# Optimization experiments

Measured on AMD Instinct MI355X. Metric: run time of the kernel, lower is better.

## Reference

```python
import jax, jax.numpy as jnp
import numpy as np

B, T, C = 512, 256, 384   # batch, seq (== block_size), n_embd
HS, BS = 64, 256          # head_size, block_size


def setup_inputs() -> dict:
    key = jax.random.key(0)
    ks = jax.random.split(key, 6)
    s = 1.0 / np.sqrt(C)
    s2 = 1.0 / np.sqrt(HS)
    return {
        "x": jax.random.normal(ks[0], (B, T, C), jnp.float32),
        "W_q": jax.random.normal(ks[1], (C, HS), jnp.float32) * s,
        "W_k": jax.random.normal(ks[2], (C, HS), jnp.float32) * s,
        "W_v": jax.random.normal(ks[3], (C, HS), jnp.float32) * s,
        "W_ql": jax.random.normal(ks[4], (HS, BS), jnp.float32) * s2,
        "W_kl": jax.random.normal(ks[5], (HS, BS), jnp.float32) * s2,
    }


def reference(x, W_q, W_k, W_v, W_ql, W_kl):
    # One head of self-attention, additive (tanh) score variant, eval mode.
    # x: [B,T,C]
    q = jnp.einsum("btc,ch->bth", x, W_q)          # [B,T,HS]
    k = jnp.einsum("btc,ch->bth", x, W_k)          # [B,T,HS]
    q_w = jnp.einsum("bth,hs->bts", q, W_ql)       # [B,T,BS]
    k_w = jnp.einsum("bth,hs->bts", k, W_kl)       # [B,T,BS]
    # NOTE: elementwise add (both [B,T,BS]) as in the torch code, then tanh.
    wei = jnp.tanh(q_w + k_w)                      # [B,T,T] since T == BS
    Tn = x.shape[1]
    causal = jnp.tril(jnp.ones((Tn, Tn), dtype=bool))
    wei = jnp.where(causal, wei, -jnp.inf)
    wei = jax.nn.softmax(wei, axis=-1)
    v = jnp.einsum("btc,ch->bth", x, W_v)          # [B,T,HS]
    out = jnp.einsum("bts,bsh->bth", wei, v)       # [B,T,HS]
    return out
```

## Files before the change

kernel.cpp:

```cpp
#include <hip/hip_runtime.h>

#define BATCH 512
#define TT    256
#define CC    384
#define HH    64

typedef float  f32x4 __attribute__((ext_vector_type(4)));
typedef short  s16x8 __attribute__((ext_vector_type(8)));

#define VB_OFF    0
#define SCR_OFF   32768
#define LDS_TOTAL 131072

__device__ __forceinline__ unsigned short f2bf(float f) {
    union { float f; unsigned u; } c; c.f = f;
    unsigned u = c.u;
    u += 0x7fffu + ((u >> 16) & 1u);
    return (unsigned short)(u >> 16);
}

__device__ __forceinline__ s16x8 cvt8(float4 f0, float4 f1) {
    s16x8 v;
    v[0] = (short)f2bf(f0.x); v[1] = (short)f2bf(f0.y);
    v[2] = (short)f2bf(f0.z); v[3] = (short)f2bf(f0.w);
    v[4] = (short)f2bf(f1.x); v[5] = (short)f2bf(f1.y);
    v[6] = (short)f2bf(f1.z); v[7] = (short)f2bf(f1.w);
    return v;
}

__global__ void prep_w(const float* __restrict__ Wq, const float* __restrict__ Wk,
                       const float* __restrict__ Wv, const float* __restrict__ Wql,
                       const float* __restrict__ Wkl, unsigned short* __restrict__ wsW) {
    int gid = blockIdx.x * 256 + threadIdx.x;
    int k, n; float val;
    if (gid < CC * 256) {
        k = gid >> 8; int s = gid & 255; n = s;
        float acc = 0.f;
        for (int h = 0; h < HH; ++h)
            acc += Wq[k * HH + h] * Wql[h * 256 + s] + Wk[k * HH + h] * Wkl[h * 256 + s];
        val = acc;
    } else {
        int g2 = gid - CC * 256;
        k = g2 >> 6; int h = g2 & 63; n = 256 + h;
        val = Wv[k * HH + h];
    }
    int kk2 = k >> 5, ct = n >> 4;
    int lane = ((k >> 3) & 3) * 16 + (n & 15);
    int j = k & 7;
    wsW[(((kk2 * 20 + ct) * 64) + lane) * 8 + j] = f2bf(val);
}

__global__ __launch_bounds__(512, 2) void head_main(const float* __restrict__ x,
                                                    const unsigned short* __restrict__ wsW,
                                                    float* __restrict__ out) {
    extern __shared__ char sm[];
    unsigned short* Vb  = (unsigned short*)(sm + VB_OFF);

    const int t    = threadIdx.x;
    const int w    = (t >> 6) & 7;
    const int lane = t & 63;
    const int q    = lane >> 4;
    const int cidx = lane & 15;
    const int rt0  = w;
    const int rt1  = 15 - w;
    unsigned short* scr = (unsigned short*)(sm + SCR_OFF + w * 12288);

    const float* xb  = x + (size_t)blockIdx.x * (TT * CC);
    const float* xa0 = xb + (rt0 * 16 + cidx) * CC + q * 8;
    const float* xa1 = xb + (rt1 * 16 + cidx) * CC + q * 8;

    f32x4 accV[2][4];
#pragma unroll
    for (int i = 0; i < 2; ++i)
#pragma unroll
        for (int j = 0; j < 4; ++j) accV[i][j] = (f32x4){0.f,0.f,0.f,0.f};
    {
        float4 p00 = *(const float4*)(xa0),     p01 = *(const float4*)(xa0 + 4);
        float4 p10 = *(const float4*)(xa1),     p11 = *(const float4*)(xa1 + 4);
        for (int kk = 0; kk < 12; ++kk) {
            s16x8 a0 = cvt8(p00, p01), a1 = cvt8(p10, p11);
            if (kk < 11) {
                const float* n0 = xa0 + (kk + 1) * 32;
                const float* n1 = xa1 + (kk + 1) * 32;
                p00 = *(const float4*)(n0); p01 = *(const float4*)(n0 + 4);
                p10 = *(const float4*)(n1); p11 = *(const float4*)(n1 + 4);
            }
            const unsigned short* wb = wsW + (size_t)kk * 10240 + 16 * 512 + lane * 8;
            s16x8 b0 = *(const s16x8*)(wb);
            s16x8 b1 = *(const s16x8*)(wb + 512);
            s16x8 b2 = *(const s16x8*)(wb + 1024);
            s16x8 b3 = *(const s16x8*)(wb + 1536);
            accV[0][0] = __builtin_amdgcn_mfma_f32_16x16x32_bf16(a0, b0, accV[0][0], 0, 0, 0);
            accV[1][0] = __builtin_amdgcn_mfma_f32_16x16x32_bf16(a1, b0, accV[1][0], 0, 0, 0);
            accV[0][1] = __builtin_amdgcn_mfma_f32_16x16x32_bf16(a0, b1, accV[0][1], 0, 0, 0);
            accV[1][1] = __builtin_amdgcn_mfma_f32_16x16x32_bf16(a1, b1, accV[1][1], 0, 0, 0);
            accV[0][2] = __builtin_amdgcn_mfma_f32_16x16x32_bf16(a0, b2, accV[0][2], 0, 0, 0);
            accV[1][2] = __builtin_amdgcn_mfma_f32_16x16x32_bf16(a1, b2, accV[1][2], 0, 0, 0);
            accV[0][3] = __builtin_amdgcn_mfma_f32_16x16x32_bf16(a0, b3, accV[0][3], 0, 0, 0);
            accV[1][3] = __builtin_amdgcn_mfma_f32_16x16x32_bf16(a1, b3, accV[1][3], 0, 0, 0);
        }
    }
#pragma unroll
    for (int ri = 0; ri < 2; ++ri) {
        const int rt = ri ? rt1 : rt0;
#pragma unroll
        for (int vct = 0; vct < 4; ++vct)
#pragma unroll
            for (int rg = 0; rg < 4; ++rg) {
                int srow = rt * 16 + q * 4 + rg;
                Vb[((vct * 8 + (srow >> 5)) * 64 + ((srow >> 3) & 3) * 16 + cidx) * 8 + (srow & 7)] =
                    f2bf(accV[ri][vct][rg]);
            }
    }

    f32x4 accS1[16], accS0[8];
#pragma unroll
    for (int i = 0; i < 16; ++i) accS1[i] = (f32x4){0.f,0.f,0.f,0.f};
#pragma unroll
    for (int i = 0; i < 8; ++i)  accS0[i] = (f32x4){0.f,0.f,0.f,0.f};

    const bool ng4   = (rt1 >= 12);
    const bool g0two = (rt0 >= 4);
    {
        float4 p00 = *(const float4*)(xa0),     p01 = *(const float4*)(xa0 + 4);
        float4 p10 = *(const float4*)(xa1),     p11 = *(const float4*)(xa1 + 4);
        for (int kk = 0; kk < 12; ++kk) {
            s16x8 a0 = cvt8(p00, p01), a1 = cvt8(p10, p11);
            if (kk < 11) {
                const float* n0 = xa0 + (kk + 1) * 32;
                const float* n1 = xa1 + (kk + 1) * 32;
                p00 = *(const float4*)(n0); p01 = *(const float4*)(n0 + 4);
                p10 = *(const float4*)(n1); p11 = *(const float4*)(n1 + 4);
            }
            const unsigned short* wb = wsW + (size_t)kk * 10240 + lane * 8;
            s16x8 bfA[4], bfB[4];
#pragma unroll
            for (int i = 0; i < 4; ++i) bfA[i] = *(const s16x8*)(wb + i * 512);
#pragma unroll
            for (int i = 0; i < 4; ++i) bfB[i] = *(const s16x8*)(wb + (4 + i) * 512);
#pragma unroll
            for (int i = 0; i < 4; ++i) {
                accS1[i] = __builtin_amdgcn_mfma_f32_16x16x32_bf16(a1, bfA[i], accS1[i], 0, 0, 0);
                accS0[i] = __builtin_amdgcn_mfma_f32_16x16x32_bf16(a0, bfA[i], accS0[i], 0, 0, 0);
            }
#pragma unroll
            for (int i = 0; i < 4; ++i) bfA[i] = *(const s16x8*)(wb + (8 + i) * 512);
#pragma unroll
            for (int i = 0; i < 4; ++i)
                accS1[4 + i] = __builtin_amdgcn_mfma_f32_16x16x32_bf16(a1, bfB[i], accS1[4 + i], 0, 0, 0);
            if (g0two) {
#pragma unroll
                for (int i = 0; i < 4; ++i)
                    accS0[4 + i] = __builtin_amdgcn_mfma_f32_16x16x32_bf16(a0, bfB[i], accS0[4 + i], 0, 0, 0);
            }
            if (ng4) {
#pragma unroll
                for (int i = 0; i < 4; ++i) bfB[i] = *(const s16x8*)(wb + (12 + i) * 512);
            }
#pragma unroll
            for (int i = 0; i < 4; ++i)
                accS1[8 + i] = __builtin_amdgcn_mfma_f32_16x16x32_bf16(a1, bfA[i], accS1[8 + i], 0, 0, 0);
            if (ng4) {
#pragma unroll
                for (int i = 0; i < 4; ++i)
                    accS1[12 + i] = __builtin_amdgcn_mfma_f32_16x16x32_bf16(a1, bfB[i], accS1[12 + i], 0, 0, 0);
            }
        }
    }

    float rs0[4] = {0.f,0.f,0.f,0.f}, rs1[4] = {0.f,0.f,0.f,0.f};
    s16x8 pf0[4], pf1[8];
    const int nch1 = rt1 >> 1;
    const int nch0 = rt0 >> 1;

#pragma unroll
    for (int ch = 0; ch < 8; ++ch) {
        if (ch <= nch1) {
#pragma unroll
            for (int sub = 0; sub < 2; ++sub) {
                const int ct = 2 * ch + sub;
                const int gcol = ct * 16 + cidx;
                const int c = sub * 16 + cidx;
#pragma unroll
                for (int rg = 0; rg < 4; ++rg) {
                    const int grow = rt1 * 16 + q * 4 + rg;
                    float e = 0.f;
                    if (ct <= rt1 && gcol <= grow) {
                        float sv = accS1[ct][rg];
                        float ex = __expf(2.f * sv);
                        float th = 1.f - __fdividef(2.f, ex + 1.f);
                        e = __expf(th);
                    }
                    rs1[rg] += e;
                    scr[ch * 512 + ((c >> 3) * 16 + q * 4 + rg) * 8 + (c & 7)] = f2bf(e);
                }
            }
        }
    }
#pragma unroll
    for (int ch = 0; ch < 8; ++ch)
        if (ch <= nch1) pf1[ch] = *(const s16x8*)(scr + ch * 512 + lane * 8);

#pragma unroll
    for (int ch = 0; ch < 4; ++ch) {
        if (ch <= nch0) {
#pragma unroll
            for (int sub = 0; sub < 2; ++sub) {
                const int ct = 2 * ch + sub;
                const int gcol = ct * 16 + cidx;
                const int c = sub * 16 + cidx;
#pragma unroll
                for (int rg = 0; rg < 4; ++rg) {
                    const int grow = rt0 * 16 + q * 4 + rg;
                    float e = 0.f;
                    if (ct <= rt0 && gcol <= grow) {
                        float sv = accS0[ct][rg];
                        float ex = __expf(2.f * sv);
                        float th = 1.f - __fdividef(2.f, ex + 1.f);
                        e = __expf(th);
                    }
                    rs0[rg] += e;
                    scr[4096 + ch * 512 + ((c >> 3) * 16 + q * 4 + rg) * 8 + (c & 7)] = f2bf(e);
                }
            }
        }
    }
#pragma unroll
    for (int ch = 0; ch < 4; ++ch)
        if (ch <= nch0) pf0[ch] = *(const s16x8*)(scr + 4096 + ch * 512 + lane * 8);

#pragma unroll
    for (int rg = 0; rg < 4; ++rg) {
        float v0 = rs0[rg], v1 = rs1[rg];
        v0 += __shfl_xor(v0, 1); v0 += __shfl_xor(v0, 2);
        v0 += __shfl_xor(v0, 4); v0 += __shfl_xor(v0, 8);
        v1 += __shfl_xor(v1, 1); v1 += __shfl_xor(v1, 2);
        v1 += __shfl_xor(v1, 4); v1 += __shfl_xor(v1, 8);
        rs0[rg] = v0; rs1[rg] = v1;
    }

    __syncthreads();

    f32x4 acc2[2][4];
#pragma unroll
    for (int i = 0; i < 2; ++i)
#pragma unroll
        for (int j = 0; j < 4; ++j) acc2[i][j] = (f32x4){0.f,0.f,0.f,0.f};

#pragma unroll
    for (int ch = 0; ch < 8; ++ch) {
        if (ch <= nch1) {
            s16x8 vb[4];
#pragma unroll
            for (int vct = 0; vct < 4; ++vct)
                vb[vct] = *(const s16x8*)(Vb + ((vct * 8 + ch) * 64 + lane) * 8);
#pragma unroll
            for (int vct = 0; vct < 4; ++vct)
                acc2[1][vct] = __builtin_amdgcn_mfma_f32_16x16x32_bf16(pf1[ch], vb[vct], acc2[1][vct], 0, 0, 0);
            if (ch < 4 && ch <= nch0) {
#pragma unroll
                for (int vct = 0; vct < 4; ++vct)
                    acc2[0][vct] = __builtin_amdgcn_mfma_f32_16x16x32_bf16(pf0[ch], vb[vct], acc2[0][vct], 0, 0, 0);
            }
        }
    }

    float* ob = out + (size_t)blockIdx.x * (TT * HH);
#pragma unroll
    for (int ri = 0; ri < 2; ++ri) {
        const int rt = ri ? rt1 : rt0;
#pragma unroll
        for (int rg = 0; rg < 4; ++rg) {
            int row = rt * 16 + q * 4 + rg;
            float inv = __fdividef(1.f, ri ? rs1[rg] : rs0[rg]);
#pragma unroll
            for (int vct = 0; vct < 4; ++vct)
                ob[row * HH + vct * 16 + cidx] = acc2[ri][vct][rg] * inv;
        }
    }
}

extern "C" void kernel_launch(void* const* d_in, const int* in_sizes, int n_in,
                              void* d_out, int out_size, void* d_ws, size_t ws_size,
                              hipStream_t stream) {
    const float* x   = (const float*)d_in[0];
    const float* Wq  = (const float*)d_in[1];
    const float* Wk  = (const float*)d_in[2];
    const float* Wv  = (const float*)d_in[3];
    const float* Wql = (const float*)d_in[4];
    const float* Wkl = (const float*)d_in[5];
    unsigned short* wsW = (unsigned short*)d_ws;
    float* out = (float*)d_out;

    prep_w<<<480, 256, 0, stream>>>(Wq, Wk, Wv, Wql, Wkl, wsW);

    hipFuncSetAttribute((const void*)head_main,
                        hipFuncAttributeMaxDynamicSharedMemorySize, LDS_TOTAL);
    head_main<<<BATCH, 512, LDS_TOTAL, stream>>>(x, wsW, out);
}
```

Measured before the change: 361.4 us.

## Merge score accumulators, shrink LDS scratch, raise occupancy to four blocks per CU

Both row tiles now share one 18-entry score accumulator array, with the short row tile packed into the slots the long tile leaves unused, so fewer accumulator registers are live. Per-wave scratch shrinks to a two-slot ping-pong buffer and total LDS falls from 128KB to 48KB, so launch bounds can target four 512-thread blocks per CU. MFMAs for tiles entirely above the causal diagonal are skipped per tile. The trade-offs are more LDS round trips and possible register spills under the tighter register budget.

```diff
diff --git a/kernel.cpp b/kernel.cpp
--- a/kernel.cpp
+++ b/kernel.cpp
@@ -10,7 +10,7 @@
 
 #define VB_OFF    0
 #define SCR_OFF   32768
-#define LDS_TOTAL 131072
+#define LDS_TOTAL 49152
 
 __device__ __forceinline__ unsigned short f2bf(float f) {
     union { float f; unsigned u; } c; c.f = f;
@@ -50,7 +50,7 @@
     wsW[(((kk2 * 20 + ct) * 64) + lane) * 8 + j] = f2bf(val);
 }
 
-__global__ __launch_bounds__(512, 2) void head_main(const float* __restrict__ x,
+__global__ __launch_bounds__(512, 4) void head_main(const float* __restrict__ x,
                                                     const unsigned short* __restrict__ wsW,
                                                     float* __restrict__ out) {
     extern __shared__ char sm[];
@@ -63,7 +63,9 @@
     const int cidx = lane & 15;
     const int rt0  = w;
     const int rt1  = 15 - w;
-    unsigned short* scr = (unsigned short*)(sm + SCR_OFF + w * 12288);
+    const int nt0  = rt0 + 2 - (rt0 & 1);
+    const int jbase = 18 - nt0;
+    unsigned short* scr = (unsigned short*)(sm + SCR_OFF) + w * 1024;
 
     const float* xb  = x + (size_t)blockIdx.x * (TT * CC);
     const float* xa0 = xb + (rt0 * 16 + cidx) * CC + q * 8;
@@ -75,8 +77,8 @@
 #pragma unroll
         for (int j = 0; j < 4; ++j) accV[i][j] = (f32x4){0.f,0.f,0.f,0.f};
     {
-        float4 p00 = *(const float4*)(xa0),     p01 = *(const float4*)(xa0 + 4);
-        float4 p10 = *(const float4*)(xa1),     p11 = *(const float4*)(xa1 + 4);
+        float4 p00 = *(const float4*)(xa0), p01 = *(const float4*)(xa0 + 4);
+        float4 p10 = *(const float4*)(xa1), p11 = *(const float4*)(xa1 + 4);
         for (int kk = 0; kk < 12; ++kk) {
             s16x8 a0 = cvt8(p00, p01), a1 = cvt8(p10, p11);
             if (kk < 11) {
@@ -113,17 +115,13 @@
             }
     }
 
-    f32x4 accS1[16], accS0[8];
-#pragma unroll
-    for (int i = 0; i < 16; ++i) accS1[i] = (f32x4){0.f,0.f,0.f,0.f};
-#pragma unroll
-    for (int i = 0; i < 8; ++i)  accS0[i] = (f32x4){0.f,0.f,0.f,0.f};
-
-    const bool ng4   = (rt1 >= 12);
-    const bool g0two = (rt0 >= 4);
+    f32x4 accS[18];
+#pragma unroll
+    for (int i = 0; i < 18; ++i) accS[i] = (f32x4){0.f,0.f,0.f,0.f};
+
     {
-        float4 p00 = *(const float4*)(xa0),     p01 = *(const float4*)(xa0 + 4);
-        float4 p10 = *(const float4*)(xa1),     p11 = *(const float4*)(xa1 + 4);
+        float4 p00 = *(const float4*)(xa0), p01 = *(const float4*)(xa0 + 4);
+        float4 p10 = *(const float4*)(xa1), p11 = *(const float4*)(xa1 + 4);
         for (int kk = 0; kk < 12; ++kk) {
             s16x8 a0 = cvt8(p00, p01), a1 = cvt8(p10, p11);
             if (kk < 11) {
@@ -133,37 +131,38 @@
                 p10 = *(const float4*)(n1); p11 = *(const float4*)(n1 + 4);
             }
             const unsigned short* wb = wsW + (size_t)kk * 10240 + lane * 8;
-            s16x8 bfA[4], bfB[4];
-#pragma unroll
-            for (int i = 0; i < 4; ++i) bfA[i] = *(const s16x8*)(wb + i * 512);
-#pragma unroll
-            for (int i = 0; i < 4; ++i) bfB[i] = *(const s16x8*)(wb + (4 + i) * 512);
-#pragma unroll
-            for (int i = 0; i < 4; ++i) {
-                accS1[i] = __builtin_amdgcn_mfma_f32_16x16x32_bf16(a1, bfA[i], accS1[i], 0, 0, 0);
-                accS0[i] = __builtin_amdgcn_mfma_f32_16x16x32_bf16(a0, bfA[i], accS0[i], 0, 0, 0);
-            }
-#pragma unroll
-            for (int i = 0; i < 4; ++i) bfA[i] = *(const s16x8*)(wb + (8 + i) * 512);
+            s16x8 bf[4];
+#pragma unroll
+            for (int i = 0; i < 4; ++i) bf[i] = *(const s16x8*)(wb + i * 512);
 #pragma unroll
             for (int i = 0; i < 4; ++i)
-                accS1[4 + i] = __builtin_amdgcn_mfma_f32_16x16x32_bf16(a1, bfB[i], accS1[4 + i], 0, 0, 0);
-            if (g0two) {
+                accS[i] = __builtin_amdgcn_mfma_f32_16x16x32_bf16(a1, bf[i], accS[i], 0, 0, 0);
+#pragma unroll
+            for (int i = 0; i < 4; ++i) bf[i] = *(const s16x8*)(wb + (4 + i) * 512);
+#pragma unroll
+            for (int i = 0; i < 4; ++i)
+                accS[4 + i] = __builtin_amdgcn_mfma_f32_16x16x32_bf16(a1, bf[i], accS[4 + i], 0, 0, 0);
+#pragma unroll
+            for (int i = 0; i < 4; ++i) bf[i] = *(const s16x8*)(wb + (8 + i) * 512);
+#pragma unroll
+            for (int i = 0; i < 4; ++i)
+                if (8 + i <= rt1)
+                    accS[8 + i] = __builtin_amdgcn_mfma_f32_16x16x32_bf16(a1, bf[i], accS[8 + i], 0, 0, 0);
+            if (rt1 >= 12) {
+#pragma unroll
+                for (int i = 0; i < 4; ++i) bf[i] = *(const s16x8*)(wb + (12 + i) * 512);
 #pragma unroll
                 for (int i = 0; i < 4; ++i)
-                    accS0[4 + i] = __builtin_amdgcn_mfma_f32_16x16x32_bf16(a0, bfB[i], accS0[4 + i], 0, 0, 0);
-            }
-            if (ng4) {
-#pragma unroll
-                for (int i = 0; i < 4; ++i) bfB[i] = *(const s16x8*)(wb + (12 + i) * 512);
-            }
-#pragma unroll
-            for (int i = 0; i < 4; ++i)
-                accS1[8 + i] = __builtin_amdgcn_mfma_f32_16x16x32_bf16(a1, bfA[i], accS1[8 + i], 0, 0, 0);
-            if (ng4) {
-#pragma unroll
-                for (int i = 0; i < 4; ++i)
-                    accS1[12 + i] = __builtin_amdgcn_mfma_f32_16x16x32_bf16(a1, bfB[i], accS1[12 + i], 0, 0, 0);
+                    if (12 + i <= rt1)
+                        accS[12 + i] = __builtin_amdgcn_mfma_f32_16x16x32_bf16(a1, bf[i], accS[12 + i], 0, 0, 0);
+            }
+            const unsigned short* wb0 = wb - jbase * 512;
+#pragma unroll
+            for (int j = 10; j < 18; ++j) {
+                if (j >= jbase) {
+                    s16x8 b = *(const s16x8*)(wb0 + j * 512);
+                    accS[j] = __builtin_amdgcn_mfma_f32_16x16x32_bf16(a0, b, accS[j], 0, 0, 0);
+                }
             }
         }
     }
@@ -171,11 +170,11 @@
     float rs0[4] = {0.f,0.f,0.f,0.f}, rs1[4] = {0.f,0.f,0.f,0.f};
     s16x8 pf0[4], pf1[8];
     const int nch1 = rt1 >> 1;
-    const int nch0 = rt0 >> 1;
 
 #pragma unroll
     for (int ch = 0; ch < 8; ++ch) {
         if (ch <= nch1) {
+            unsigned short* reg = scr + (ch & 1) * 512;
 #pragma unroll
             for (int sub = 0; sub < 2; ++sub) {
                 const int ct = 2 * ch + sub;
@@ -186,48 +185,46 @@
                     const int grow = rt1 * 16 + q * 4 + rg;
                     float e = 0.f;
                     if (ct <= rt1 && gcol <= grow) {
-                        float sv = accS1[ct][rg];
+                        float sv = accS[ct][rg];
                         float ex = __expf(2.f * sv);
                         float th = 1.f - __fdividef(2.f, ex + 1.f);
                         e = __expf(th);
                     }
                     rs1[rg] += e;
-                    scr[ch * 512 + ((c >> 3) * 16 + q * 4 + rg) * 8 + (c & 7)] = f2bf(e);
+                    reg[((c >> 3) * 16 + q * 4 + rg) * 8 + (c & 7)] = f2bf(e);
                 }
             }
-        }
-    }
-#pragma unroll
-    for (int ch = 0; ch < 8; ++ch)
-        if (ch <= nch1) pf1[ch] = *(const s16x8*)(scr + ch * 512 + lane * 8);
-
-#pragma unroll
-    for (int ch = 0; ch < 4; ++ch) {
-        if (ch <= nch0) {
+            pf1[ch] = *(const s16x8*)(reg + lane * 8);
+        }
+    }
+#pragma unroll
+    for (int s = 0; s < 4; ++s) {
+        const int je = 10 + 2 * s;
+        if (je >= jbase) {
+            const int ch0 = (je - jbase) >> 1;
+            unsigned short* reg = scr + (s & 1) * 512;
 #pragma unroll
             for (int sub = 0; sub < 2; ++sub) {
-                const int ct = 2 * ch + sub;
-                const int gcol = ct * 16 + cidx;
+                const int ct0 = 2 * ch0 + sub;
+                const int gcol = ct0 * 16 + cidx;
                 const int c = sub * 16 + cidx;
 #pragma unroll
                 for (int rg = 0; rg < 4; ++rg) {
                     const int grow = rt0 * 16 + q * 4 + rg;
                     float e = 0.f;
-                    if (ct <= rt0 && gcol <= grow) {
-                        float sv = accS0[ct][rg];
+                    if (ct0 <= rt0 && gcol <= grow) {
+                        float sv = accS[je + sub][rg];
                         float ex = __expf(2.f * sv);
                         float th = 1.f - __fdividef(2.f, ex + 1.f);
                         e = __expf(th);
                     }
                     rs0[rg] += e;
-                    scr[4096 + ch * 512 + ((c >> 3) * 16 + q * 4 + rg) * 8 + (c & 7)] = f2bf(e);
+                    reg[((c >> 3) * 16 + q * 4 + rg) * 8 + (c & 7)] = f2bf(e);
                 }
             }
-        }
-    }
-#pragma unroll
-    for (int ch = 0; ch < 4; ++ch)
-        if (ch <= nch0) pf0[ch] = *(const s16x8*)(scr + 4096 + ch * 512 + lane * 8);
+            pf0[s] = *(const s16x8*)(reg + lane * 8);
+        }
+    }
 
 #pragma unroll
     for (int rg = 0; rg < 4; ++rg) {
@@ -257,11 +254,19 @@
 #pragma unroll
             for (int vct = 0; vct < 4; ++vct)
                 acc2[1][vct] = __builtin_amdgcn_mfma_f32_16x16x32_bf16(pf1[ch], vb[vct], acc2[1][vct], 0, 0, 0);
-            if (ch < 4 && ch <= nch0) {
-#pragma unroll
-                for (int vct = 0; vct < 4; ++vct)
-                    acc2[0][vct] = __builtin_amdgcn_mfma_f32_16x16x32_bf16(pf0[ch], vb[vct], acc2[0][vct], 0, 0, 0);
-            }
+        }
+    }
+#pragma unroll
+    for (int s = 0; s < 4; ++s) {
+        if (10 + 2 * s >= jbase) {
+            const int ch0 = s - ((jbase - 10) >> 1);
+            s16x8 vb[4];
+#pragma unroll
+            for (int vct = 0; vct < 4; ++vct)
+                vb[vct] = *(const s16x8*)(Vb + ((vct * 8 + ch0) * 64 + lane) * 8);
+#pragma unroll
+            for (int vct = 0; vct < 4; ++vct)
+                acc2[0][vct] = __builtin_amdgcn_mfma_f32_16x16x32_bf16(pf0[s], vb[vct], acc2[0][vct], 0, 0, 0);
         }
     }
 
@@ -294,7 +299,5 @@
 
     prep_w<<<480, 256, 0, stream>>>(Wq, Wk, Wv, Wql, Wkl, wsW);
 
-    hipFuncSetAttribute((const void*)head_main,
-                        hipFuncAttributeMaxDynamicSharedMemorySize, LDS_TOTAL);
     head_main<<<BATCH, 512, LDS_TOTAL, stream>>>(x, wsW, out);
 }
```

Result: slower. 386.8 us (+7.0%).
